# Optimization experiments

Hardware: AMD Instinct MI355X
Metric: run time of the kernel (lower is better)

Reference implementation:

```python
import jax, jax.numpy as jnp
import numpy as np

DIM = 256
WINDOW = 512  # look_backward=1, look_forward=0, causal


def setup_inputs() -> dict:
    key = jax.random.key(0)
    ks = jax.random.split(key, 7)
    B, N, D = 8, 8192, DIM
    s = D ** -0.5
    return {
        "x": jax.random.normal(ks[0], (B, D, N), dtype=jnp.float32),
        "Wq": jax.random.normal(ks[1], (D, D), dtype=jnp.float32) * s,
        "bq": jax.random.normal(ks[2], (D,), dtype=jnp.float32) * 0.01,
        "Wk": jax.random.normal(ks[3], (D, D), dtype=jnp.float32) * s,
        "bk": jax.random.normal(ks[4], (D,), dtype=jnp.float32) * 0.01,
        "Wv": jax.random.normal(ks[5], (D, D), dtype=jnp.float32) * s,
        "bv": jax.random.normal(ks[6], (D,), dtype=jnp.float32) * 0.01,
    }


def _local_attention(q, k, v, window):
    # q,k,v: (B, N, D); causal sliding-window attention, look_backward=1 window.
    b, n, d = q.shape
    nw = n // window  # N assumed multiple of window (autopad no-op here)
    scale = d ** -0.5
    qb = q.reshape(b, nw, window, d)
    kb = k.reshape(b, nw, window, d)
    vb = v.reshape(b, nw, window, d)

    def look_back(t):
        prev = jnp.pad(t, ((0, 0), (1, 0), (0, 0), (0, 0)))[:, :-1]
        return jnp.concatenate([prev, t], axis=2)  # (b, nw, 2*window, d)

    kb2 = look_back(kb)
    vb2 = look_back(vb)

    pos = jnp.arange(n).reshape(nw, window)
    prev_pos = jnp.pad(pos, ((1, 0), (0, 0)), constant_values=-1)[:-1]
    kpos = jnp.concatenate([prev_pos, pos], axis=1)  # (nw, 2*window)
    # causal mask + mask out the (nonexistent) window before window 0
    mask = (pos[:, :, None] >= kpos[:, None, :]) & (kpos[:, None, :] >= 0)

    scores = jnp.einsum('bnqd,bnkd->bnqk', qb, kb2) * scale
    scores = jnp.where(mask[None], scores, jnp.asarray(-1e9, scores.dtype))
    attn = jax.nn.softmax(scores, axis=-1)  # dropout(0.1) omitted: eval mode
    out = jnp.einsum('bnqk,bnkd->bnqd', attn, vb2)
    return out.reshape(b, n, d)


def reference(x, Wq, bq, Wk, bk, Wv, bv):
    # x: (B, D, N) -> permute -> (B, N, D)
    xp = jnp.transpose(x, (0, 2, 1))
    q = xp @ Wq.T + bq
    k = xp @ Wk.T + bk
    v = xp @ Wv.T + bv
    y = xp + _local_attention(q, k, v, WINDOW)  # residual
    return jnp.transpose(y, (0, 2, 1))
```

## Files before the change

### kernel.cpp

```cpp
#include <hip/hip_runtime.h>
#include <hip/hip_bf16.h>

#define DIM  256
#define NSEQ 8192
#define BATCH 8
#define WIN  512

typedef __attribute__((ext_vector_type(8))) short short8;
typedef __attribute__((ext_vector_type(4))) float floatx4;

union PFU { int i[4]; short8 v; };

__device__ __forceinline__ int packbf(float a, float b) {
    __hip_bfloat162 h;
    h.x = __float2bfloat16(a);
    h.y = __float2bfloat16(b);
    int r;
    __builtin_memcpy(&r, &h, 4);
    return r;
}

__device__ __forceinline__ void gld_lds16(void* lds_dst, const void* g_src) {
    __builtin_amdgcn_global_load_lds(
        (const __attribute__((address_space(1))) void*)g_src,
        (__attribute__((address_space(3))) void*)lds_dst,
        16, 0, 0);
}

__global__ __launch_bounds__(256) void k_transpose(const float* __restrict__ x,
                                                   __hip_bfloat16* __restrict__ xT) {
    __shared__ float tile[64][65];
    const int b  = blockIdx.z;
    const int n0 = blockIdx.x * 64;
    const int d0 = blockIdx.y * 64;
    const int t  = threadIdx.x;
    const int ln = t & 63, grp = t >> 6;

    const float* xb = x + (size_t)b * DIM * NSEQ;
#pragma unroll
    for (int i = 0; i < 16; ++i) {
        int d = grp * 16 + i;
        tile[d][ln] = xb[(size_t)(d0 + d) * NSEQ + n0 + ln];
    }
    __syncthreads();
    __hip_bfloat16* xTb = xT + (size_t)b * NSEQ * DIM;
#pragma unroll
    for (int i = 0; i < 16; ++i) {
        int n = grp * 16 + i;
        xTb[(size_t)(n0 + n) * DIM + d0 + ln] = __float2bfloat16(tile[ln][n]);
    }
}

__global__ __launch_bounds__(256) void k_wcast(const float* __restrict__ w0,
                                               const float* __restrict__ w1,
                                               const float* __restrict__ w2,
                                               __hip_bfloat16* __restrict__ wb) {
    int i = (blockIdx.x * 256 + threadIdx.x) * 4;
    const float* s = (i < 65536) ? (w0 + i) : ((i < 131072) ? (w1 + i - 65536) : (w2 + i - 131072));
    float4 v = *(const float4*)s;
    union { __hip_bfloat16 h[4]; ushort4 u; } cv;
    cv.h[0] = __float2bfloat16(v.x);
    cv.h[1] = __float2bfloat16(v.y);
    cv.h[2] = __float2bfloat16(v.z);
    cv.h[3] = __float2bfloat16(v.w);
    *(ushort4*)(wb + i) = cv.u;
}

__global__ __launch_bounds__(256) void k_proj(const __hip_bfloat16* __restrict__ xT,
                                              const __hip_bfloat16* __restrict__ wb,
                                              const float* __restrict__ bq,
                                              const float* __restrict__ bk,
                                              const float* __restrict__ bv,
                                              __hip_bfloat16* __restrict__ qo,
                                              __hip_bfloat16* __restrict__ ko,
                                              __hip_bfloat16* __restrict__ vto) {
    __shared__ __hip_bfloat16 As[4096];
    __shared__ __hip_bfloat16 Bs[4096];

    const int mode = blockIdx.y;
    const int b    = blockIdx.z;
    const int xb   = blockIdx.x;
    const int tid  = threadIdx.x;
    const int wv   = tid >> 6;
    const int l    = tid & 63;
    const int qd   = l >> 4;
    const int lm   = l & 15;
    const int wm   = (wv & 1) * 64;
    const int wn   = (wv >> 1) * 64;

    int m0, n0;
    const __hip_bfloat16 *Ap, *Bp;
    const __hip_bfloat16* xTb = xT + (size_t)b * NSEQ * DIM;
    if (mode < 2) {
        m0 = (xb >> 1) * 128;  n0 = (xb & 1) * 128;
        Ap = xTb + (size_t)m0 * DIM;
        Bp = wb + mode * 65536 + (size_t)n0 * DIM;
    } else {
        m0 = (xb & 1) * 128;   n0 = (xb >> 1) * 128;
        Ap = wb + 2 * 65536 + (size_t)m0 * DIM;
        Bp = xTb + (size_t)n0 * DIM;
    }

    floatx4 acc[4][4];
#pragma unroll
    for (int i = 0; i < 4; ++i)
#pragma unroll
        for (int j = 0; j < 4; ++j) acc[i][j] = (floatx4){0.f, 0.f, 0.f, 0.f};

    for (int k0 = 0; k0 < DIM; k0 += 32) {
#pragma unroll
        for (int r = 0; r < 2; ++r) {
            int row = r * 64 + (tid >> 2);
            int seg = (tid & 3) * 8;
            gld_lds16((char*)As + r * 4096 + wv * 1024, Ap + (size_t)row * DIM + k0 + seg);
            gld_lds16((char*)Bs + r * 4096 + wv * 1024, Bp + (size_t)row * DIM + k0 + seg);
        }
        __syncthreads();
        short8 af[4], bfv[4];
#pragma unroll
        for (int mt = 0; mt < 4; ++mt)
            af[mt] = *(const short8*)(As + (wm + mt * 16 + lm) * 32 + qd * 8);
#pragma unroll
        for (int nt = 0; nt < 4; ++nt)
            bfv[nt] = *(const short8*)(Bs + (wn + nt * 16 + lm) * 32 + qd * 8);
#pragma unroll
        for (int mt = 0; mt < 4; ++mt)
#pragma unroll
            for (int nt = 0; nt < 4; ++nt)
                acc[mt][nt] = __builtin_amdgcn_mfma_f32_16x16x32_bf16(af[mt], bfv[nt], acc[mt][nt], 0, 0, 0);
        __syncthreads();
    }

    const float* bias = (mode == 0) ? bq : ((mode == 1) ? bk : bv);
    __hip_bfloat16* op;
    size_t ostr;
    if (mode == 0)      { op = qo  + (size_t)b * NSEQ * DIM; ostr = DIM; }
    else if (mode == 1) { op = ko  + (size_t)b * NSEQ * DIM; ostr = DIM; }
    else                { op = vto + (size_t)b * DIM * NSEQ; ostr = NSEQ; }

    float bc[4];
    if (mode < 2) {
#pragma unroll
        for (int nt = 0; nt < 4; ++nt) bc[nt] = bias[n0 + wn + nt * 16 + lm];
    }
#pragma unroll
    for (int mt = 0; mt < 4; ++mt)
#pragma unroll
        for (int nt = 0; nt < 4; ++nt)
#pragma unroll
            for (int r = 0; r < 4; ++r) {
                int row = wm + mt * 16 + qd * 4 + r;
                int col = wn + nt * 16 + lm;
                float bb = (mode < 2) ? bc[nt] : bias[m0 + row];
                op[(size_t)(m0 + row) * ostr + n0 + col] = __float2bfloat16(acc[mt][nt][r] + bb);
            }
}

__global__ __launch_bounds__(512, 2) void k_attn(const __hip_bfloat16* __restrict__ qm,
                                                 const __hip_bfloat16* __restrict__ km,
                                                 const __hip_bfloat16* __restrict__ vtm,
                                                 const float* __restrict__ x,
                                                 float* __restrict__ out) {
    __shared__ __align__(16) char kbuf[2][16384];
    __shared__ __align__(16) char vbuf[2][16384];

    const int w  = blockIdx.x, b = blockIdx.y, qt = blockIdx.z;
    const int tid = threadIdx.x;
    const int wv = tid >> 6;
    const int l  = tid & 63;
    const int m  = l & 15;
    const int qd = l >> 4;

    const int qb    = qt * 128 + wv * 16;
    const int koff0 = w * WIN - WIN;

    const __hip_bfloat16* qrow = qm + ((size_t)b * NSEQ + (size_t)(w * WIN + qb + m)) * DIM;
    short8 qf[8];
#pragma unroll
    for (int s = 0; s < 8; ++s)
        qf[s] = *(const short8*)(qrow + s * 32 + qd * 8);

    const char* kbase = (const char*)(km + (size_t)b * NSEQ * DIM);
    const char* vbase = (const char*)(vtm + (size_t)b * DIM * NSEQ);

    const int c0  = (w == 0) ? 16 : 0;
    const int c1w = (512 + qb + 47) >> 5;
    const int c1b = (671 + qt * 128) >> 5;

    const bool   isK     = wv < 4;
    const size_t gstride = isK ? (size_t)64 : (size_t)16 * NSEQ * 2;
    const size_t adv     = isK ? (size_t)32 * 512 : (size_t)64;
    const int    lbase   = (isK ? wv * 4 : (wv - 4) * 4) * 1024 + l * 16;
    const char* gp0;
    if (isK)
        gp0 = kbase + (size_t)(koff0 + c0 * 32 + (wv >> 1) * 16 + m) * 512 +
              (size_t)((wv & 1) * 16 + qd) * 16;
    else
        gp0 = vbase + (size_t)((wv - 4) * 64 + m) * (NSEQ * 2) +
              (size_t)(koff0 + c0 * 32) * 2 + (size_t)qd * 16;

    floatx4 o[16];
#pragma unroll
    for (int t = 0; t < 16; ++t) o[t] = (floatx4){0.f, 0.f, 0.f, 0.f};
    float mi = -INFINITY, li = 0.f;
    const int lim = 512 + qb + m;
    const float sscale = 0.0625f * 1.4426950408889634f;

    const int a0 = (((qd & 1) * 2) * 16 + m) * 4;
    const int a1 = a0 + 64;
    const bool hi = (qd >> 1) != 0;

    int4 rg[4];
#pragma unroll
    for (int i = 0; i < 4; ++i)
        rg[i] = *(const int4*)(gp0 + (size_t)i * gstride);
    gp0 += adv;
    {
        char* d0 = (isK ? kbuf[0] : vbuf[0]) + lbase;
#pragma unroll
        for (int i = 0; i < 4; ++i)
            *(int4*)(d0 + i * 1024) = rg[i];
    }
    __syncthreads();

    int pb = 0;
    for (int c = c0; c < c1b; ++c) {
        const bool more = (c + 1 < c1b);
        if (more) {
#pragma unroll
            for (int i = 0; i < 4; ++i)
                rg[i] = *(const int4*)(gp0 + (size_t)i * gstride);
            gp0 += adv;
        }
        if (c < c1w) {
            const char* kbp = kbuf[pb];
            floatx4 st[2];
#pragma unroll
            for (int t = 0; t < 2; ++t) {
                floatx4 a = (floatx4){0.f, 0.f, 0.f, 0.f};
#pragma unroll
                for (int s = 0; s < 8; ++s) {
                    short8 kf = *(const short8*)(kbp + ((t * 8 + s) * 64 + l) * 16);
                    a = __builtin_amdgcn_mfma_f32_16x16x32_bf16(kf, qf[s], a, 0, 0, 0);
                }
                st[t] = a;
            }
            const int kl0 = c * 32;
            const bool needmask = (kl0 + 31) > lim;
            float p[8];
#pragma unroll
            for (int t = 0; t < 2; ++t)
#pragma unroll
                for (int r = 0; r < 4; ++r) {
                    float v = st[t][r] * sscale;
                    if (needmask) {
                        int key = kl0 + t * 16 + qd * 4 + r;
                        v = (key <= lim) ? v : -INFINITY;
                    }
                    p[t * 4 + r] = v;
                }
            float mx = p[0];
#pragma unroll
            for (int i = 1; i < 8; ++i) mx = fmaxf(mx, p[i]);
            mx = fmaxf(mx, __shfl_xor(mx, 16, 64));
            mx = fmaxf(mx, __shfl_xor(mx, 32, 64));
            const float mnew  = fmaxf(mi, mx);
            const float alpha = exp2f(mi - mnew);
            float ps = 0.f;
#pragma unroll
            for (int i = 0; i < 8; ++i) { p[i] = exp2f(p[i] - mnew); ps += p[i]; }
            ps += __shfl_xor(ps, 16, 64);
            ps += __shfl_xor(ps, 32, 64);
            li = li * alpha + ps;
            mi = mnew;
#pragma unroll
            for (int t = 0; t < 16; ++t) {
                o[t][0] *= alpha; o[t][1] *= alpha; o[t][2] *= alpha; o[t][3] *= alpha;
            }
            int pd0 = packbf(p[0], p[1]);
            int pd1 = packbf(p[2], p[3]);
            int pd2 = packbf(p[4], p[5]);
            int pd3 = packbf(p[6], p[7]);
            int x0 = __builtin_amdgcn_ds_bpermute(a0, pd0);
            int y0 = __builtin_amdgcn_ds_bpermute(a0, pd2);
            int x1 = __builtin_amdgcn_ds_bpermute(a0, pd1);
            int y1 = __builtin_amdgcn_ds_bpermute(a0, pd3);
            int x2 = __builtin_amdgcn_ds_bpermute(a1, pd0);
            int y2 = __builtin_amdgcn_ds_bpermute(a1, pd2);
            int x3 = __builtin_amdgcn_ds_bpermute(a1, pd1);
            int y3 = __builtin_amdgcn_ds_bpermute(a1, pd3);
            PFU u;
            u.i[0] = hi ? y0 : x0;
            u.i[1] = hi ? y1 : x1;
            u.i[2] = hi ? y2 : x2;
            u.i[3] = hi ? y3 : x3;
            short8 pf = u.v;
            const char* vbp = vbuf[pb];
#pragma unroll
            for (int t = 0; t < 16; ++t) {
                short8 vf = *(const short8*)(vbp + (t * 64 + l) * 16);
                o[t] = __builtin_amdgcn_mfma_f32_16x16x32_bf16(vf, pf, o[t], 0, 0, 0);
            }
        }
        if (more) {
            char* dst = (isK ? kbuf[pb ^ 1] : vbuf[pb ^ 1]) + lbase;
#pragma unroll
            for (int i = 0; i < 4; ++i)
                *(int4*)(dst + i * 1024) = rg[i];
        }
        __syncthreads();
        pb ^= 1;
    }

    const float inv = 1.f / li;
    const int ng = w * WIN + qb + m;
    const float* xr  = x   + (size_t)b * DIM * NSEQ + ng;
    float*       orw = out + (size_t)b * DIM * NSEQ + ng;
#pragma unroll
    for (int t = 0; t < 16; ++t)
#pragma unroll
        for (int r = 0; r < 4; ++r) {
            int d = t * 16 + qd * 4 + r;
            orw[(size_t)d * NSEQ] = xr[(size_t)d * NSEQ] + o[t][r] * inv;
        }
}

extern "C" void kernel_launch(void* const* d_in, const int* in_sizes, int n_in,
                              void* d_out, int out_size, void* d_ws, size_t ws_size,
                              hipStream_t stream) {
    const float* x  = (const float*)d_in[0];
    const float* Wq = (const float*)d_in[1];
    const float* bq = (const float*)d_in[2];
    const float* Wk = (const float*)d_in[3];
    const float* bk = (const float*)d_in[4];
    const float* Wv = (const float*)d_in[5];
    const float* bv = (const float*)d_in[6];

    char* ws = (char*)d_ws;
    const size_t SZ = (size_t)BATCH * NSEQ * DIM * sizeof(__hip_bfloat16);
    __hip_bfloat16* xT  = (__hip_bfloat16*)(ws);
    __hip_bfloat16* qb_ = (__hip_bfloat16*)(ws + SZ);
    __hip_bfloat16* kb_ = (__hip_bfloat16*)(ws + 2 * SZ);
    __hip_bfloat16* vt_ = (__hip_bfloat16*)(ws + 3 * SZ);
    __hip_bfloat16* wb_ = (__hip_bfloat16*)(ws + 4 * SZ);

    k_transpose<<<dim3(NSEQ / 64, DIM / 64, BATCH), 256, 0, stream>>>(x, xT);
    k_wcast<<<dim3(192), 256, 0, stream>>>(Wq, Wk, Wv, wb_);
    k_proj<<<dim3(128, 3, BATCH), 256, 0, stream>>>(xT, wb_, bq, bk, bv, qb_, kb_, vt_);
    k_attn<<<dim3(16, BATCH, 4), 512, 0, stream>>>(qb_, kb_, vt_, x, (float*)d_out);
}
```

Before: 372.4 us.

## Process two 16-row query tiles per wave to reuse K/V LDS fragments

Each wave now owns 32 query rows, split into two 16-row sub-tiles. Every K and V fragment read from LDS feeds two MFMAs, and the number of query-tile blocks is halved, so each K/V tile is loaded from global memory fewer times. This doubles the accumulator registers per wave (o[2][16]), which risks spills or lower occupancy under launch_bounds(512,2), and the grid shrinks to 256 blocks. It also skips the output rescale when alpha is 1 across the whole wave.

```diff
diff --git a/kernel.cpp b/kernel.cpp
--- a/kernel.cpp
+++ b/kernel.cpp
@@ -171,21 +171,25 @@
     const int m  = l & 15;
     const int qd = l >> 4;
 
-    const int qb    = qt * 128 + wv * 16;
+    const int qbw   = qt * 256 + wv * 32;
     const int koff0 = w * WIN - WIN;
 
-    const __hip_bfloat16* qrow = qm + ((size_t)b * NSEQ + (size_t)(w * WIN + qb + m)) * DIM;
-    short8 qf[8];
-#pragma unroll
-    for (int s = 0; s < 8; ++s)
-        qf[s] = *(const short8*)(qrow + s * 32 + qd * 8);
+    short8 qf[2][8];
+#pragma unroll
+    for (int u = 0; u < 2; ++u) {
+        const __hip_bfloat16* qrow =
+            qm + ((size_t)b * NSEQ + (size_t)(w * WIN + qbw + u * 16 + m)) * DIM;
+#pragma unroll
+        for (int s = 0; s < 8; ++s)
+            qf[u][s] = *(const short8*)(qrow + s * 32 + qd * 8);
+    }
 
     const char* kbase = (const char*)(km + (size_t)b * NSEQ * DIM);
     const char* vbase = (const char*)(vtm + (size_t)b * DIM * NSEQ);
 
     const int c0  = (w == 0) ? 16 : 0;
-    const int c1w = (512 + qb + 47) >> 5;
-    const int c1b = (671 + qt * 128) >> 5;
+    const int c1w = (512 + qbw + 63) >> 5;
+    const int c1b = (799 + qt * 256) >> 5;
 
     const bool   isK     = wv < 4;
     const size_t gstride = isK ? (size_t)64 : (size_t)16 * NSEQ * 2;
@@ -199,11 +203,13 @@
         gp0 = vbase + (size_t)((wv - 4) * 64 + m) * (NSEQ * 2) +
               (size_t)(koff0 + c0 * 32) * 2 + (size_t)qd * 16;
 
-    floatx4 o[16];
-#pragma unroll
-    for (int t = 0; t < 16; ++t) o[t] = (floatx4){0.f, 0.f, 0.f, 0.f};
-    float mi = -INFINITY, li = 0.f;
-    const int lim = 512 + qb + m;
+    floatx4 o[2][16];
+#pragma unroll
+    for (int u = 0; u < 2; ++u)
+#pragma unroll
+        for (int t = 0; t < 16; ++t) o[u][t] = (floatx4){0.f, 0.f, 0.f, 0.f};
+    float mi[2] = {-INFINITY, -INFINITY};
+    float li[2] = {0.f, 0.f};
     const float sscale = 0.0625f * 1.4426950408889634f;
 
     const int a0 = (((qd & 1) * 2) * 16 + m) * 4;
@@ -234,72 +240,83 @@
         }
         if (c < c1w) {
             const char* kbp = kbuf[pb];
-            floatx4 st[2];
-#pragma unroll
-            for (int t = 0; t < 2; ++t) {
-                floatx4 a = (floatx4){0.f, 0.f, 0.f, 0.f};
+            floatx4 st[2][2];
+#pragma unroll
+            for (int u = 0; u < 2; ++u)
+#pragma unroll
+                for (int t = 0; t < 2; ++t) st[u][t] = (floatx4){0.f, 0.f, 0.f, 0.f};
+#pragma unroll
+            for (int t = 0; t < 2; ++t)
 #pragma unroll
                 for (int s = 0; s < 8; ++s) {
                     short8 kf = *(const short8*)(kbp + ((t * 8 + s) * 64 + l) * 16);
-                    a = __builtin_amdgcn_mfma_f32_16x16x32_bf16(kf, qf[s], a, 0, 0, 0);
+                    st[0][t] = __builtin_amdgcn_mfma_f32_16x16x32_bf16(kf, qf[0][s], st[0][t], 0, 0, 0);
+                    st[1][t] = __builtin_amdgcn_mfma_f32_16x16x32_bf16(kf, qf[1][s], st[1][t], 0, 0, 0);
                 }
-                st[t] = a;
+            const int kl0 = c * 32;
+            short8 pf[2];
+#pragma unroll
+            for (int u = 0; u < 2; ++u) {
+                const int lim = 512 + qbw + u * 16 + m;
+                const bool needmask = (kl0 + 31) > lim;
+                float p[8];
+#pragma unroll
+                for (int t = 0; t < 2; ++t)
+#pragma unroll
+                    for (int r = 0; r < 4; ++r) {
+                        float v = st[u][t][r] * sscale;
+                        if (needmask) {
+                            int key = kl0 + t * 16 + qd * 4 + r;
+                            v = (key <= lim) ? v : -INFINITY;
+                        }
+                        p[t * 4 + r] = v;
+                    }
+                float mx = p[0];
+#pragma unroll
+                for (int i = 1; i < 8; ++i) mx = fmaxf(mx, p[i]);
+                mx = fmaxf(mx, __shfl_xor(mx, 16, 64));
+                mx = fmaxf(mx, __shfl_xor(mx, 32, 64));
+                const float mnew  = fmaxf(mi[u], mx);
+                const float alpha = exp2f(mi[u] - mnew);
+                float ps = 0.f;
+#pragma unroll
+                for (int i = 0; i < 8; ++i) { p[i] = exp2f(p[i] - mnew); ps += p[i]; }
+                ps += __shfl_xor(ps, 16, 64);
+                ps += __shfl_xor(ps, 32, 64);
+                li[u] = li[u] * alpha + ps;
+                mi[u] = mnew;
+                if (!__all(alpha == 1.0f)) {
+#pragma unroll
+                    for (int t = 0; t < 16; ++t) {
+                        o[u][t][0] *= alpha; o[u][t][1] *= alpha;
+                        o[u][t][2] *= alpha; o[u][t][3] *= alpha;
+                    }
+                }
+                int pd0 = packbf(p[0], p[1]);
+                int pd1 = packbf(p[2], p[3]);
+                int pd2 = packbf(p[4], p[5]);
+                int pd3 = packbf(p[6], p[7]);
+                int x0 = __builtin_amdgcn_ds_bpermute(a0, pd0);
+                int y0 = __builtin_amdgcn_ds_bpermute(a0, pd2);
+                int x1 = __builtin_amdgcn_ds_bpermute(a0, pd1);
+                int y1 = __builtin_amdgcn_ds_bpermute(a0, pd3);
+                int x2 = __builtin_amdgcn_ds_bpermute(a1, pd0);
+                int y2 = __builtin_amdgcn_ds_bpermute(a1, pd2);
+                int x3 = __builtin_amdgcn_ds_bpermute(a1, pd1);
+                int y3 = __builtin_amdgcn_ds_bpermute(a1, pd3);
+                PFU pu;
+                pu.i[0] = hi ? y0 : x0;
+                pu.i[1] = hi ? y1 : x1;
+                pu.i[2] = hi ? y2 : x2;
+                pu.i[3] = hi ? y3 : x3;
+                pf[u] = pu.v;
             }
-            const int kl0 = c * 32;
-            const bool needmask = (kl0 + 31) > lim;
-            float p[8];
-#pragma unroll
-            for (int t = 0; t < 2; ++t)
-#pragma unroll
-                for (int r = 0; r < 4; ++r) {
-                    float v = st[t][r] * sscale;
-                    if (needmask) {
-                        int key = kl0 + t * 16 + qd * 4 + r;
-                        v = (key <= lim) ? v : -INFINITY;
-                    }
-                    p[t * 4 + r] = v;
-                }
-            float mx = p[0];
-#pragma unroll
-            for (int i = 1; i < 8; ++i) mx = fmaxf(mx, p[i]);
-            mx = fmaxf(mx, __shfl_xor(mx, 16, 64));
-            mx = fmaxf(mx, __shfl_xor(mx, 32, 64));
-            const float mnew  = fmaxf(mi, mx);
-            const float alpha = exp2f(mi - mnew);
-            float ps = 0.f;
-#pragma unroll
-            for (int i = 0; i < 8; ++i) { p[i] = exp2f(p[i] - mnew); ps += p[i]; }
-            ps += __shfl_xor(ps, 16, 64);
-            ps += __shfl_xor(ps, 32, 64);
-            li = li * alpha + ps;
-            mi = mnew;
-#pragma unroll
-            for (int t = 0; t < 16; ++t) {
-                o[t][0] *= alpha; o[t][1] *= alpha; o[t][2] *= alpha; o[t][3] *= alpha;
-            }
-            int pd0 = packbf(p[0], p[1]);
-            int pd1 = packbf(p[2], p[3]);
-            int pd2 = packbf(p[4], p[5]);
-            int pd3 = packbf(p[6], p[7]);
-            int x0 = __builtin_amdgcn_ds_bpermute(a0, pd0);
-            int y0 = __builtin_amdgcn_ds_bpermute(a0, pd2);
-            int x1 = __builtin_amdgcn_ds_bpermute(a0, pd1);
-            int y1 = __builtin_amdgcn_ds_bpermute(a0, pd3);
-            int x2 = __builtin_amdgcn_ds_bpermute(a1, pd0);
-            int y2 = __builtin_amdgcn_ds_bpermute(a1, pd2);
-            int x3 = __builtin_amdgcn_ds_bpermute(a1, pd1);
-            int y3 = __builtin_amdgcn_ds_bpermute(a1, pd3);
-            PFU u;
-            u.i[0] = hi ? y0 : x0;
-            u.i[1] = hi ? y1 : x1;
-            u.i[2] = hi ? y2 : x2;
-            u.i[3] = hi ? y3 : x3;
-            short8 pf = u.v;
             const char* vbp = vbuf[pb];
 #pragma unroll
             for (int t = 0; t < 16; ++t) {
                 short8 vf = *(const short8*)(vbp + (t * 64 + l) * 16);
-                o[t] = __builtin_amdgcn_mfma_f32_16x16x32_bf16(vf, pf, o[t], 0, 0, 0);
+                o[0][t] = __builtin_amdgcn_mfma_f32_16x16x32_bf16(vf, pf[0], o[0][t], 0, 0, 0);
+                o[1][t] = __builtin_amdgcn_mfma_f32_16x16x32_bf16(vf, pf[1], o[1][t], 0, 0, 0);
             }
         }
         if (more) {
@@ -312,17 +329,20 @@
         pb ^= 1;
     }
 
-    const float inv = 1.f / li;
-    const int ng = w * WIN + qb + m;
-    const float* xr  = x   + (size_t)b * DIM * NSEQ + ng;
-    float*       orw = out + (size_t)b * DIM * NSEQ + ng;
-#pragma unroll
-    for (int t = 0; t < 16; ++t)
-#pragma unroll
-        for (int r = 0; r < 4; ++r) {
-            int d = t * 16 + qd * 4 + r;
-            orw[(size_t)d * NSEQ] = xr[(size_t)d * NSEQ] + o[t][r] * inv;
-        }
+#pragma unroll
+    for (int u = 0; u < 2; ++u) {
+        const float inv = 1.f / li[u];
+        const int ng = w * WIN + qbw + u * 16 + m;
+        const float* xr  = x   + (size_t)b * DIM * NSEQ + ng;
+        float*       orw = out + (size_t)b * DIM * NSEQ + ng;
+#pragma unroll
+        for (int t = 0; t < 16; ++t)
+#pragma unroll
+            for (int r = 0; r < 4; ++r) {
+                int d = t * 16 + qd * 4 + r;
+                orw[(size_t)d * NSEQ] = xr[(size_t)d * NSEQ] + o[u][t][r] * inv;
+            }
+    }
 }
 
 extern "C" void kernel_launch(void* const* d_in, const int* in_sizes, int n_in,
@@ -347,5 +367,5 @@
     k_transpose<<<dim3(NSEQ / 64, DIM / 64, BATCH), 256, 0, stream>>>(x, xT);
     k_wcast<<<dim3(192), 256, 0, stream>>>(Wq, Wk, Wv, wb_);
     k_proj<<<dim3(128, 3, BATCH), 256, 0, stream>>>(xT, wb_, bq, bk, bv, qb_, kb_, vt_);
-    k_attn<<<dim3(16, BATCH, 4), 512, 0, stream>>>(qb_, kb_, vt_, x, (float*)d_out);
-}
+    k_attn<<<dim3(16, BATCH, 2), 512, 0, stream>>>(qb_, kb_, vt_, x, (float*)d_out);
+}
```

New measurement: 354.1 us. -4.9%, faster.
